# Performance work log

Hardware: AMD Instinct MI355X
Metric: run time of the kernel (lower is better)

Reference implementation:

```python
import jax, jax.numpy as jnp
import numpy as np

INPUT_SIZE = 40960
HIDDEN = 256
MAX_FEATS = 32
BATCH = 8192


def setup_inputs() -> dict:
    key = jax.random.key(0)
    ks = jax.random.split(key, 10)
    wf = jax.random.randint(ks[0], (BATCH, MAX_FEATS), 0, INPUT_SIZE, dtype=jnp.int64 if jax.config.jax_enable_x64 else jnp.int32)
    bf = jax.random.randint(ks[1], (BATCH, MAX_FEATS), 0, INPUT_SIZE, dtype=wf.dtype)
    pad_w = jax.random.uniform(ks[2], (BATCH, MAX_FEATS)) < 0.25
    pad_b = jax.random.uniform(ks[3], (BATCH, MAX_FEATS)) < 0.25
    wf = jnp.where(pad_w, -1, wf)
    bf = jnp.where(pad_b, -1, bf)
    stm = jax.random.bernoulli(ks[4], 0.5, (BATCH,)).astype(jnp.float32)
    # Parameters (torch Linear convention: weight [out, in]).
    bound = 1.0 / np.sqrt(INPUT_SIZE)
    ft_W = jax.random.uniform(ks[5], (HIDDEN, INPUT_SIZE), jnp.float32, -bound, bound)
    ft_b = jnp.zeros((HIDDEN,), jnp.float32)
    w1 = jax.random.normal(ks[6], (32, HIDDEN * 2), jnp.float32) * np.sqrt(2.0 / (HIDDEN * 2))
    b1 = jnp.zeros((32,), jnp.float32)
    w2 = jax.random.normal(ks[7], (32, 32), jnp.float32) * np.sqrt(2.0 / 32)
    b2 = jnp.zeros((32,), jnp.float32)
    wo = jax.random.uniform(ks[8], (1, 32), jnp.float32, -0.1, 0.1)
    bo = jnp.zeros((1,), jnp.float32)
    return {"white_features": wf, "black_features": bf, "stm": stm,
            "ft_W": ft_W, "ft_b": ft_b, "w1": w1, "b1": b1,
            "w2": w2, "b2": b2, "wo": wo, "bo": bo}


def _accumulate(idx, ft_Wt, ft_b):
    # idx: [B, F] with -1 padding; ft_Wt: [INPUT_SIZE, HIDDEN]
    valid = (idx >= 0)
    idxc = jnp.clip(idx, 0, INPUT_SIZE - 1)
    g = ft_Wt[idxc] * valid[..., None].astype(ft_Wt.dtype)  # [B, F, H]
    return g.sum(axis=1) + ft_b  # [B, H]


def reference(white_features, black_features, stm, ft_W, ft_b, w1, b1, w2, b2, wo, bo):
    ft_Wt = ft_W.T  # [INPUT_SIZE, HIDDEN]
    wh = _accumulate(white_features, ft_Wt, ft_b)
    bh = _accumulate(black_features, ft_Wt, ft_b)
    # clamp(relu(x), 0, 127) == clip(x, 0, 127)
    wh = jnp.clip(wh, 0.0, 127.0)
    bh = jnp.clip(bh, 0.0, 127.0)
    s = stm[:, None]
    us = s * wh + (1.0 - s) * bh
    them = s * bh + (1.0 - s) * wh
    x = jnp.concatenate([us, them], axis=1)  # [B, 2H]
    x = jax.nn.relu(x @ w1.T + b1)
    x = jax.nn.relu(x @ w2.T + b2)
    x = x @ wo.T + bo  # [B, 1]
    return jax.nn.sigmoid(x.squeeze(-1))
```

## Files before the change

kernel.cpp:

```cpp
#include <hip/hip_runtime.h>
#include <math.h>

#define BATCH   8192
#define HIDDEN  256
#define MAXF    32
#define ISZ     40960
#define TF2     32

#define QSCALE  7.842927e-5f
#define INVQ    1.2750335e+4f
#define QOFF    (4096.0f * QSCALE)

#define SEL_EVEN 0x00060004u
#define SEL_ODD  0x00070005u

__global__ __launch_bounds__(256) void transpose_q32(const float* __restrict__ src,
                                                     unsigned char* __restrict__ dstq,
                                                     const float* __restrict__ w1,
                                                     const float* __restrict__ w2,
                                                     float* __restrict__ w1c,
                                                     float* __restrict__ w2t) {
    unsigned int* dq = (unsigned int*)dstq;

    if (blockIdx.x == ISZ / TF2) {
        for (int i = threadIdx.x; i < 32 * 512; i += 256) {
            int j = i >> 9, k = i & 511;
            w1c[(k >> 2) * 128 + j * 4 + (k & 3)] = w1[i];
        }
        for (int i = threadIdx.x; i < 32 * 32; i += 256) {
            int j = i >> 5, k = i & 31;
            w2t[k * 32 + j] = w2[i];
        }
        if (threadIdx.x < 64)
            dq[(size_t)ISZ * 64 + threadIdx.x] = 0x80808080u;
        return;
    }

    __shared__ short tile[TF2][260];
    const int t    = threadIdx.x;
    const int wave = t >> 6;
    const int lane = t & 63;
    const int F0   = blockIdx.x * TF2;

#pragma unroll
    for (int i = 0; i < 8; ++i) {
        const int h  = i * 32 + wave * 8 + (lane >> 3);
        const int fb = 4 * (lane & 7);
        const float4 v = *(const float4*)&src[(size_t)h * ISZ + F0 + fb];
        int q0 = __float2int_rn(v.x * INVQ); q0 = max(-127, min(127, q0)) + 128;
        int q1 = __float2int_rn(v.y * INVQ); q1 = max(-127, min(127, q1)) + 128;
        int q2 = __float2int_rn(v.z * INVQ); q2 = max(-127, min(127, q2)) + 128;
        int q3 = __float2int_rn(v.w * INVQ); q3 = max(-127, min(127, q3)) + 128;
        tile[fb + 0][h] = (short)q0;
        tile[fb + 1][h] = (short)q1;
        tile[fb + 2][h] = (short)q2;
        tile[fb + 3][h] = (short)q3;
    }
    __syncthreads();

#pragma unroll
    for (int f = wave; f < TF2; f += 4) {
        const short4 q = *(const short4*)&tile[f][4 * lane];
        unsigned int p = (q.x & 0xFF) | ((q.y & 0xFF) << 8) |
                         ((q.z & 0xFF) << 16) | ((unsigned int)(q.w & 0xFF) << 24);
        dq[(size_t)(F0 + f) * 64 + lane] = p;
    }
}

__global__ __launch_bounds__(256) void nnue_fused_q(
    const int* __restrict__ wf, const int* __restrict__ bfeat,
    const float* __restrict__ stm,
    const unsigned char* __restrict__ ftQ,
    const float* __restrict__ ftb,
    const float* __restrict__ w1c, const float* __restrict__ b1,
    const float* __restrict__ w2,  const float* __restrict__ b2,
    const float* __restrict__ wo,  const float* __restrict__ bo,
    float* __restrict__ out) {

    __shared__ int   sIdx[4][32][4];
    __shared__ float sX[8][512];
    __shared__ float sY1[8][32];
    __shared__ float sY2[8][32];

    const int t    = threadIdx.x;
    const int wave = t >> 6;
    const int lane = t & 63;
    const int g    = lane >> 4;
    const int c16  = lane & 15;
    const int ib0  = blockIdx.x * 8;

    {
        const int item = t >> 5, f = t & 31;
        sIdx[item >> 1][f][(item & 1) * 2 + 0] = wf   [(ib0 + item) * MAXF + f];
        sIdx[item >> 1][f][(item & 1) * 2 + 1] = bfeat[(ib0 + item) * MAXF + f];
    }
    __syncthreads();

    unsigned acc[8];
#pragma unroll
    for (int k = 0; k < 8; ++k) acc[k] = 0u;

    const uint4* Tl = (const uint4*)ftQ + c16;

#pragma unroll
    for (int fb = 0; fb < 4; ++fb) {
        uint4 d[8];
#pragma unroll
        for (int u = 0; u < 8; ++u) {
            const int idx = sIdx[wave][fb * 8 + u][g];
            const int rc  = idx < 0 ? ISZ : idx;
            d[u] = Tl[(size_t)rc * 16];
        }
#pragma unroll
        for (int u = 0; u < 8; ++u) {
            acc[0] += __builtin_amdgcn_perm(d[u].x, 0u, SEL_EVEN);
            acc[1] += __builtin_amdgcn_perm(d[u].x, 0u, SEL_ODD);
            acc[2] += __builtin_amdgcn_perm(d[u].y, 0u, SEL_EVEN);
            acc[3] += __builtin_amdgcn_perm(d[u].y, 0u, SEL_ODD);
            acc[4] += __builtin_amdgcn_perm(d[u].z, 0u, SEL_EVEN);
            acc[5] += __builtin_amdgcn_perm(d[u].z, 0u, SEL_ODD);
            acc[6] += __builtin_amdgcn_perm(d[u].w, 0u, SEL_EVEN);
            acc[7] += __builtin_amdgcn_perm(d[u].w, 0u, SEL_ODD);
        }
    }

    const float4* ftb4 = (const float4*)ftb;
    float h[16];
#pragma unroll
    for (int m = 0; m < 4; ++m) {
        const float4 tb = ftb4[c16 * 4 + m];
        h[4*m+0] = (float)(acc[2*m]     & 0xFFFFu) * QSCALE + (tb.x - QOFF);
        h[4*m+1] = (float)(acc[2*m + 1] & 0xFFFFu) * QSCALE + (tb.y - QOFF);
        h[4*m+2] = (float)(acc[2*m]    >> 16)      * QSCALE + (tb.z - QOFF);
        h[4*m+3] = (float)(acc[2*m + 1] >> 16)     * QSCALE + (tb.w - QOFF);
    }
#pragma unroll
    for (int u = 0; u < 16; ++u) h[u] = fminf(fmaxf(h[u], 0.f), 127.f);

    const int   li  = wave * 2 + (g >> 1);
    const float s   = stm[ib0 + li];
    const int   off = (((g & 1) == 0) == (s > 0.5f)) ? 0 : 256;
    float* xrow = &sX[li][off + 16 * c16];
#pragma unroll
    for (int m = 0; m < 4; ++m)
        *(float4*)&xrow[4 * m] = make_float4(h[4*m], h[4*m+1], h[4*m+2], h[4*m+3]);
    __syncthreads();

    {
        const int j = t & 31, q = t >> 5;
        const float4* w1c4 = (const float4*)w1c;
        float y = b1[j];
#pragma unroll 4
        for (int ks = 0; ks < 128; ++ks) {
            const float4 x4 = *(const float4*)&sX[q][4 * ks];
            const float4 wv = w1c4[ks * 32 + j];
            y = fmaf(x4.x, wv.x, y); y = fmaf(x4.y, wv.y, y);
            y = fmaf(x4.z, wv.z, y); y = fmaf(x4.w, wv.w, y);
        }
        sY1[q][j] = fmaxf(y, 0.0f);
    }
    __syncthreads();

    {
        const int j = t & 31, q = t >> 5;
        float y = b2[j];
#pragma unroll
        for (int k = 0; k < 32; ++k) y = fmaf(sY1[q][k], w2[k * 32 + j], y);
        sY2[q][j] = fmaxf(y, 0.0f);
    }
    __syncthreads();

    if (t < 8) {
        float y = bo[0];
#pragma unroll
        for (int k = 0; k < 32; ++k) y = fmaf(sY2[t][k], wo[k], y);
        out[ib0 + t] = 1.0f / (1.0f + expf(-y));
    }
}

__global__ __launch_bounds__(256) void nnue_fused_fb(
    const int* __restrict__ wf, const int* __restrict__ bfeat,
    const float* __restrict__ stm,
    const float* __restrict__ ftW, const float* __restrict__ ftb,
    const float* __restrict__ w1, const float* __restrict__ b1,
    const float* __restrict__ w2, const float* __restrict__ b2,
    const float* __restrict__ wo, const float* __restrict__ bo,
    float* __restrict__ out) {

    __shared__ float sX[4][512];
    __shared__ float sP[2][4][32];
    __shared__ float sY2[4][32];

    const int t = threadIdx.x, wave = t >> 6, lane = t & 63;
    const int b = blockIdx.x * 4 + wave;
    int myidx = (lane < 32) ? wf[b * MAXF + lane] : bfeat[b * MAXF + (lane - 32)];
    const float4* ftb4 = (const float4*)ftb;
    float4 accw = ftb4[lane];
    float4 accb = accw;

    for (int f = 0; f < MAXF; ++f) {
        int iw = __builtin_amdgcn_readlane(myidx, f);
        int ib = __builtin_amdgcn_readlane(myidx, f + 32);
        float mw = (iw >= 0) ? 1.0f : 0.0f;
        float mb = (ib >= 0) ? 1.0f : 0.0f;
        int iwc = iw < 0 ? 0 : iw;
        int ibc = ib < 0 ? 0 : ib;
#pragma unroll
        for (int c = 0; c < 4; ++c) {
            float gw = ftW[(size_t)(4 * lane + c) * ISZ + iwc];
            float gb = ftW[(size_t)(4 * lane + c) * ISZ + ibc];
            float* aw = (c == 0) ? &accw.x : (c == 1) ? &accw.y : (c == 2) ? &accw.z : &accw.w;
            float* ab = (c == 0) ? &accb.x : (c == 1) ? &accb.y : (c == 2) ? &accb.z : &accb.w;
            *aw = fmaf(gw, mw, *aw);
            *ab = fmaf(gb, mb, *ab);
        }
    }
#pragma unroll
    for (int c = 0; c < 4; ++c) {
        float* aw = (c == 0) ? &accw.x : (c == 1) ? &accw.y : (c == 2) ? &accw.z : &accw.w;
        float* ab = (c == 0) ? &accb.x : (c == 1) ? &accb.y : (c == 2) ? &accb.z : &accb.w;
        *aw = fminf(fmaxf(*aw, 0.f), 127.f);
        *ab = fminf(fmaxf(*ab, 0.f), 127.f);
    }
    float s = stm[b];
    float4 us, th;
    if (s > 0.5f) { us = accw; th = accb; } else { us = accb; th = accw; }
    ((float4*)sX[wave])[lane] = us;
    ((float4*)sX[wave])[64 + lane] = th;
    __syncthreads();
    {
        const int j = t & 31, q = (t >> 5) & 3, kh = t >> 7;
        const float* x = sX[q];
        float y = kh ? 0.0f : b1[j];
        const int k0 = kh * 256;
        for (int kk = 0; kk < 256; ++kk) {
            const int k = k0 + kk;
            y = fmaf(x[k], w1[j * 512 + k], y);
        }
        sP[kh][q][j] = y;
    }
    __syncthreads();
    if (t < 128) {
        const int q = t >> 5, j = t & 31;
        float y = b2[j];
        for (int k = 0; k < 32; ++k) {
            float x1 = fmaxf(sP[0][q][k] + sP[1][q][k], 0.0f);
            y = fmaf(x1, w2[j * 32 + k], y);
        }
        sY2[q][j] = fmaxf(y, 0.0f);
    }
    __syncthreads();
    if (t < 4) {
        float y = bo[0];
        for (int k = 0; k < 32; ++k) y = fmaf(sY2[t][k], wo[k], y);
        out[blockIdx.x * 4 + t] = 1.0f / (1.0f + expf(-y));
    }
}

extern "C" void kernel_launch(void* const* d_in, const int* in_sizes, int n_in,
                              void* d_out, int out_size, void* d_ws, size_t ws_size,
                              hipStream_t stream) {
    const int*   wf  = (const int*)d_in[0];
    const int*   bfe = (const int*)d_in[1];
    const float* stm = (const float*)d_in[2];
    const float* ftW = (const float*)d_in[3];
    const float* ftb = (const float*)d_in[4];
    const float* w1  = (const float*)d_in[5];
    const float* b1  = (const float*)d_in[6];
    const float* w2  = (const float*)d_in[7];
    const float* b2  = (const float*)d_in[8];
    const float* wo  = (const float*)d_in[9];
    const float* bo  = (const float*)d_in[10];
    float* out = (float*)d_out;

    const size_t ftQ_bytes = (size_t)(ISZ + 1) * HIDDEN;
    const size_t w1c_bytes = 512 * 32 * 4;
    const size_t w2t_bytes = 32 * 32 * 4;
    const size_t need      = ftQ_bytes + w1c_bytes + w2t_bytes;

    if (ws_size >= need) {
        unsigned char* ftQ = (unsigned char*)d_ws;
        float* w1c = (float*)((char*)d_ws + ftQ_bytes);
        float* w2t = w1c + 512 * 32;
        transpose_q32<<<ISZ / TF2 + 1, 256, 0, stream>>>(ftW, ftQ, w1, w2, w1c, w2t);
        nnue_fused_q<<<BATCH / 8, 256, 0, stream>>>(
            wf, bfe, stm, ftQ, ftb, w1c, b1, w2t, b2, wo, bo, out);
    } else {
        nnue_fused_fb<<<BATCH / 4, 256, 0, stream>>>(
            wf, bfe, stm, ftW, ftb, w1, b1, w2, b2, wo, bo, out);
    }
}
```

Before: 133.9 us.

## Split layer-1 GEMV across K chunks with weight reuse over 8 items; deepen gather batching

The first dense layer is repartitioned so each thread owns a slice of the K dimension and reuses each loaded w1 float4 across all 8 batch items in the block. Partial sums go to a new shared buffer and are reduced in an extra pass, which adds a barrier and some LDS traffic. Each thread previously reloaded the full w1 column per item, so global and L2 weight loads per block fall by about 8x. The feature gather also issues 16 loads per batch instead of 8 and uses 32-bit byte-offset addressing, raising memory-level parallelism at the cost of more live registers.

```diff
diff --git a/kernel.cpp b/kernel.cpp
--- a/kernel.cpp
+++ b/kernel.cpp
@@ -79,6 +79,7 @@
 
     __shared__ int   sIdx[4][32][4];
     __shared__ float sX[8][512];
+    __shared__ float sP[8][8][32];
     __shared__ float sY1[8][32];
     __shared__ float sY2[8][32];
 
@@ -100,19 +101,20 @@
 #pragma unroll
     for (int k = 0; k < 8; ++k) acc[k] = 0u;
 
-    const uint4* Tl = (const uint4*)ftQ + c16;
-
-#pragma unroll
-    for (int fb = 0; fb < 4; ++fb) {
-        uint4 d[8];
-#pragma unroll
-        for (int u = 0; u < 8; ++u) {
-            const int idx = sIdx[wave][fb * 8 + u][g];
-            const int rc  = idx < 0 ? ISZ : idx;
-            d[u] = Tl[(size_t)rc * 16];
-        }
-#pragma unroll
-        for (int u = 0; u < 8; ++u) {
+    const char* ftQb = (const char*)ftQ;
+    const unsigned lo16 = (unsigned)(c16 << 4);
+
+#pragma unroll
+    for (int fb = 0; fb < 2; ++fb) {
+        uint4 d[16];
+#pragma unroll
+        for (int u = 0; u < 16; ++u) {
+            const int idx = sIdx[wave][fb * 16 + u][g];
+            const unsigned rc = idx < 0 ? (unsigned)ISZ : (unsigned)idx;
+            d[u] = *(const uint4*)(ftQb + ((rc << 8) + lo16));
+        }
+#pragma unroll
+        for (int u = 0; u < 16; ++u) {
             acc[0] += __builtin_amdgcn_perm(d[u].x, 0u, SEL_EVEN);
             acc[1] += __builtin_amdgcn_perm(d[u].x, 0u, SEL_ODD);
             acc[2] += __builtin_amdgcn_perm(d[u].y, 0u, SEL_EVEN);
@@ -147,16 +149,32 @@
     __syncthreads();
 
     {
+        const int j = t & 31, kc = t >> 5;
+        const float4* w1c4 = (const float4*)w1c;
+        float y[8];
+#pragma unroll
+        for (int q = 0; q < 8; ++q) y[q] = 0.0f;
+#pragma unroll 4
+        for (int i = 0; i < 16; ++i) {
+            const int k4 = kc * 16 + i;
+            const float4 wv = w1c4[k4 * 32 + j];
+#pragma unroll
+            for (int q = 0; q < 8; ++q) {
+                const float4 x4 = *(const float4*)&sX[q][4 * k4];
+                y[q] = fmaf(x4.x, wv.x, y[q]); y[q] = fmaf(x4.y, wv.y, y[q]);
+                y[q] = fmaf(x4.z, wv.z, y[q]); y[q] = fmaf(x4.w, wv.w, y[q]);
+            }
+        }
+#pragma unroll
+        for (int q = 0; q < 8; ++q) sP[kc][q][j] = y[q];
+    }
+    __syncthreads();
+
+    {
         const int j = t & 31, q = t >> 5;
-        const float4* w1c4 = (const float4*)w1c;
         float y = b1[j];
-#pragma unroll 4
-        for (int ks = 0; ks < 128; ++ks) {
-            const float4 x4 = *(const float4*)&sX[q][4 * ks];
-            const float4 wv = w1c4[ks * 32 + j];
-            y = fmaf(x4.x, wv.x, y); y = fmaf(x4.y, wv.y, y);
-            y = fmaf(x4.z, wv.z, y); y = fmaf(x4.w, wv.w, y);
-        }
+#pragma unroll
+        for (int kc = 0; kc < 8; ++kc) y += sP[kc][q][j];
         sY1[q][j] = fmaxf(y, 0.0f);
     }
     __syncthreads();
```

New measurement: 127.1 us. 1.05x faster.
